# Kernel tuning notes

Measured on AMD Instinct MI355X. Metric: run time of the kernel, lower is better.

## Reference

```python
import jax, jax.numpy as jnp
import numpy as np
import math

TAU = 0.04
BIG = 100000.0


def _decay(initial, step, steps):
    de = initial * 0.75 * (1.0 + math.cos(math.pi * step / (steps / 2.0)))
    dm = initial * 0.75 * (1.0 + math.cos(math.pi * step / steps))
    e = de if step < steps / 2.0 else 0.0
    m = dm
    return e, m, 3.0 - e - m


def _normalize(x):
    return x / jnp.maximum(jnp.linalg.norm(x, axis=1, keepdims=True), 1e-12)


def _pdist(a2, b2, ab):
    # ||a_i||^2 + ||b_j||^2 - 2 a_i.b_j, clamped + sqrt (matches torch addmm_ path)
    return jnp.sqrt(jnp.clip(a2 + b2.T - 2.0 * ab, 1e-12, None))


def _row_extreme(masked, is_min):
    idx = jnp.argmin(masked, axis=1) if is_min else jnp.argmax(masked, axis=1)
    val = jnp.take_along_axis(masked, idx[:, None], axis=1)[:, 0]
    return val, idx


def _nanmedian(vals, mask):
    # lower-median over valid entries per row (torch.nanmedian semantics)
    k = mask.sum(axis=1)
    pos = jnp.maximum((k - 1) // 2, 0)
    order = jnp.argsort(jnp.where(mask, vals, jnp.inf), axis=1)
    med_idx = jnp.take_along_axis(order, pos[:, None], axis=1)[:, 0]
    med_val = jnp.take_along_axis(vals, med_idx[:, None], axis=1)[:, 0]
    med_val = jnp.where(k > 0, med_val, 0.0)  # NaN-median -> 0 as in source
    return med_val, med_idx


def _ce0(logits):
    # CrossEntropy with labels all 0 over 2 classes
    return jnp.mean(jax.nn.logsumexp(logits, axis=1) - logits[:, 0])


def _pair_loss(dist_vals_an, dist_vals_ap, an_t, ap_t):
    sg = jax.lax.stop_gradient
    w_an = jnp.clip(sg(an_t) - sg(dist_vals_an), 0.0, None)
    w_ap = jnp.clip(sg(dist_vals_ap) - sg(ap_t), 0.0, None)
    logits = jnp.stack([w_an * dist_vals_an / TAU, w_ap * dist_vals_ap / TAU], axis=1)
    return _ce0(logits)


def _forward(teacher_inputs, inputs, epoch):
    e, m, d = _decay(0.5, epoch, 240)
    t = _normalize(teacher_inputs)
    s = _normalize(inputs)
    t2 = jnp.sum(t * t, axis=1, keepdims=True)  # [n,1]
    s2 = jnp.sum(s * s, axis=1, keepdims=True)
    dist_t = _pdist(t2, t2, t @ t.T)            # teacher-teacher [n,n]
    dist = _pdist(t2, s2, t @ s.T)              # teacher-student [n,n]
    temp1 = jnp.diag(dist)[:, None]             # dist[i,i] broadcast over row i
    neg_mask = dist_t > temp1
    pos_mask = ~neg_mask

    gather_t = lambda idx: jnp.take_along_axis(dist_t, idx[:, None], axis=1)[:, 0]

    # hard mining (d-branch): nearest negative, farthest positive
    an_v, an_i = _row_extreme(jnp.where(neg_mask, dist, BIG), True)
    ap_v, ap_i = _row_extreme(jnp.where(pos_mask, dist, 0.0), False)
    loss_d = _pair_loss(an_v, ap_v, gather_t(an_i), gather_t(ap_i))

    # easy mining (e-branch): farthest negative, nearest positive
    an_ev, an_ei = _row_extreme(jnp.where(neg_mask, dist, 0.0), False)
    ap_ev, ap_ei = _row_extreme(jnp.where(pos_mask, dist, BIG), True)
    loss_e = _pair_loss(an_ev, ap_ev, gather_t(an_ei), gather_t(ap_ei))

    # median mining (m-branch)
    an_mv, an_mi = _nanmedian(dist, neg_mask)
    ap_mv, ap_mi = _nanmedian(dist, pos_mask)
    loss_m = _pair_loss(an_mv, ap_mv, gather_t(an_mi), gather_t(ap_mi))

    return loss_e * e + loss_m * m + loss_d * d


def setup_inputs() -> dict:
    key = jax.random.key(0)
    k1, k2 = jax.random.split(key)
    n, dim = 4096, 2048
    return {
        "teacher_inputs": jax.random.normal(k1, (n, dim), dtype=jnp.float32),
        "inputs": jax.random.normal(k2, (n, dim), dtype=jnp.float32),
        "epoch": 100,
    }


def reference(teacher_inputs, inputs, epoch):
    return _forward(teacher_inputs, inputs, epoch)
```

## Files before the change

### kernel.cpp

```cpp
#include <hip/hip_runtime.h>
#include <math.h>
#include <cfloat>
#include <climits>

#define NROW 4096
#define DIM  2048
#define BIGF 100000.0f
#define BIGU 0x47C35000u

typedef float  f32x4  __attribute__((ext_vector_type(4)));
typedef __bf16 bf16x8 __attribute__((ext_vector_type(8)));
typedef unsigned short us8v __attribute__((ext_vector_type(8)));

__device__ __forceinline__ unsigned short f2bf(float x) {
    unsigned u = __float_as_uint(x);
    u += 0x7fffu + ((u >> 16) & 1u);
    return (unsigned short)(u >> 16);
}
__device__ __forceinline__ float bf2f(unsigned short h) {
    return __uint_as_float(((unsigned)h) << 16);
}

__device__ __forceinline__ void gload16(const void* g, void* lds) {
    __builtin_amdgcn_global_load_lds(
        (const __attribute__((address_space(1))) unsigned int*)g,
        (__attribute__((address_space(3))) unsigned int*)lds,
        16, 0, 0);
}

__global__ __launch_bounds__(256) void k_norm_split(const float* __restrict__ in,
    unsigned short* __restrict__ hi, unsigned short* __restrict__ lo,
    float* __restrict__ sq)
{
    int row = blockIdx.x;
    int tid = threadIdx.x;
    const float4* rp = (const float4*)(in + (size_t)row * DIM);
    float4 v0 = rp[tid * 2 + 0];
    float4 v1 = rp[tid * 2 + 1];
    float ss = v0.x*v0.x + v0.y*v0.y + v0.z*v0.z + v0.w*v0.w
             + v1.x*v1.x + v1.y*v1.y + v1.z*v1.z + v1.w*v1.w;
    #pragma unroll
    for (int off = 32; off > 0; off >>= 1) ss += __shfl_down(ss, off, 64);
    __shared__ float wsum[4];
    __shared__ float s_den;
    if ((tid & 63) == 0) wsum[tid >> 6] = ss;
    __syncthreads();
    if (tid == 0) {
        float tot = wsum[0] + wsum[1] + wsum[2] + wsum[3];
        float den = fmaxf(sqrtf(tot), 1e-12f);
        s_den = den;
        sq[row] = tot / (den * den);
    }
    __syncthreads();
    float den = s_den;
    float xs[8];
    xs[0]=v0.x/den; xs[1]=v0.y/den; xs[2]=v0.z/den; xs[3]=v0.w/den;
    xs[4]=v1.x/den; xs[5]=v1.y/den; xs[6]=v1.z/den; xs[7]=v1.w/den;
    us8v hv, lv;
    #pragma unroll
    for (int j = 0; j < 8; ++j) {
        unsigned short h = f2bf(xs[j]);
        hv[j] = h;
        lv[j] = f2bf(xs[j] - bf2f(h));
    }
    *(us8v*)&hi[(size_t)row * DIM + tid * 8] = hv;
    *(us8v*)&lo[(size_t)row * DIM + tid * 8] = lv;
}

__global__ __launch_bounds__(256, 2) void k_gemm_mfma(
    const unsigned short* __restrict__ T1, const unsigned short* __restrict__ T2,
    const unsigned short* __restrict__ S1, const unsigned short* __restrict__ S2,
    const float* __restrict__ t2v, const float* __restrict__ s2v,
    float* __restrict__ distT, float* __restrict__ distS)
{
    __shared__ __align__(16) unsigned char smem[2][24576];

    int tid = threadIdx.x;

    int orig  = blockIdx.y * gridDim.x + blockIdx.x;
    int nwg   = gridDim.x * gridDim.y;
    int cpx   = nwg >> 3;
    int swz   = (orig & 7) * cpx + (orig >> 3);
    int bx    = swz % gridDim.x;
    int by    = swz / gridDim.x;
    int m0 = by * 128, n0 = bx * 128;

    int r0   = tid >> 2;
    int cs0  = (((tid & 3) ^ ((r0 >> 1) & 3)) << 4);
    unsigned ldst = (unsigned)tid * 16;

    int l  = tid & 63;
    int w  = tid >> 6;
    int wr = w >> 1, wc = w & 1;
    int lr = l & 15;
    int kc = l >> 4;

    f32x4 acc_t[4][4], acc_s[4][4];
    #pragma unroll
    for (int m = 0; m < 4; ++m)
        #pragma unroll
        for (int n = 0; n < 4; ++n) {
            acc_t[m][n] = (f32x4)0.0f;
            acc_s[m][n] = (f32x4)0.0f;
        }

    const int NT = 192;

    auto stage = [&](int tt, unsigned char* base) {
        int sg = tt >> 6;
        int k0 = (tt & 63) << 5;
        const char* pA  = (const char*)((sg == 2) ? T2 : T1);
        const char* pBt = (const char*)((sg == 1) ? T2 : T1);
        const char* pBs = (const char*)((sg == 1) ? S2 : S1);
        size_t gA0 = ((size_t)(m0 + r0)      * DIM + k0) * 2 + cs0;
        size_t gA1 = ((size_t)(m0 + 64 + r0) * DIM + k0) * 2 + cs0;
        size_t gB0 = ((size_t)(n0 + r0)      * DIM + k0) * 2 + cs0;
        size_t gB1 = ((size_t)(n0 + 64 + r0) * DIM + k0) * 2 + cs0;
        gload16(pA  + gA0, base + ldst);
        gload16(pA  + gA1, base + 4096  + ldst);
        gload16(pBt + gB0, base + 8192  + ldst);
        gload16(pBt + gB1, base + 12288 + ldst);
        gload16(pBs + gB0, base + 16384 + ldst);
        gload16(pBs + gB1, base + 20480 + ldst);
    };

    stage(0, smem[0]);
    __syncthreads();

    int cur = 0;
    for (int t = 0; t < NT; ++t) {
        if (t + 1 < NT) stage(t + 1, smem[cur ^ 1]);

        const unsigned char* base = smem[cur];
        bf16x8 a[4], btf[4], bsf[4];
        #pragma unroll
        for (int m = 0; m < 4; ++m) {
            int ra = wr * 64 + m * 16 + lr;
            int co = ((kc ^ ((ra >> 1) & 3)) << 4);
            a[m] = *(const bf16x8*)(base + ra * 64 + co);
        }
        #pragma unroll
        for (int n = 0; n < 4; ++n) {
            int rb = wc * 64 + n * 16 + lr;
            int co = ((kc ^ ((rb >> 1) & 3)) << 4);
            btf[n] = *(const bf16x8*)(base + 8192  + rb * 64 + co);
            bsf[n] = *(const bf16x8*)(base + 16384 + rb * 64 + co);
        }
        #pragma unroll
        for (int m = 0; m < 4; ++m)
            #pragma unroll
            for (int n = 0; n < 4; ++n) {
                acc_t[m][n] = __builtin_amdgcn_mfma_f32_16x16x32_bf16(
                    a[m], btf[n], acc_t[m][n], 0, 0, 0);
                acc_s[m][n] = __builtin_amdgcn_mfma_f32_16x16x32_bf16(
                    a[m], bsf[n], acc_s[m][n], 0, 0, 0);
            }

        __syncthreads();
        cur ^= 1;
    }

    int colb = n0 + wc * 64 + lr;
    int rowb = m0 + wr * 64 + (kc << 2);
    float t2row[4][4];
    #pragma unroll
    for (int m = 0; m < 4; ++m)
        #pragma unroll
        for (int r = 0; r < 4; ++r) t2row[m][r] = t2v[rowb + m * 16 + r];
    #pragma unroll
    for (int n = 0; n < 4; ++n) {
        int col = colb + n * 16;
        float t2c = t2v[col];
        float s2c = s2v[col];
        #pragma unroll
        for (int m = 0; m < 4; ++m) {
            f32x4 ct = acc_t[m][n];
            f32x4 cs = acc_s[m][n];
            int row = rowb + m * 16;
            #pragma unroll
            for (int r = 0; r < 4; ++r) {
                size_t o = (size_t)(row + r) * NROW + col;
                distT[o] = sqrtf(fmaxf(t2row[m][r] + t2c - 2.0f * ct[r], 1e-12f));
                distS[o] = sqrtf(fmaxf(t2row[m][r] + s2c - 2.0f * cs[r], 1e-12f));
            }
        }
    }
}

__device__ inline float pair_term(float an_v, float ap_v, float an_t, float ap_t)
{
    float w_an = fmaxf(an_t - an_v, 0.f);
    float w_ap = fmaxf(ap_v - ap_t, 0.f);
    float l0 = w_an * an_v / 0.04f;
    float l1 = w_ap * ap_v / 0.04f;
    float mx = fmaxf(l0, l1);
    return mx + logf(expf(l0 - mx) + expf(l1 - mx)) - l0;
}

__device__ __forceinline__ unsigned long long wred_min64(unsigned long long v) {
    #pragma unroll
    for (int o = 32; o > 0; o >>= 1) {
        unsigned long long x = __shfl_down(v, o, 64);
        v = (x < v) ? x : v;
    }
    return v;
}
__device__ __forceinline__ unsigned long long wred_max64(unsigned long long v) {
    #pragma unroll
    for (int o = 32; o > 0; o >>= 1) {
        unsigned long long x = __shfl_down(v, o, 64);
        v = (x > v) ? x : v;
    }
    return v;
}

__device__ void radix_select_reg(const unsigned u[16], unsigned negbits,
                                 unsigned selNeg, int rank,
                                 unsigned* hist, unsigned* s_wt, unsigned* s_sel,
                                 int tid, float& val, int& idx)
{
    unsigned prefix = 0;
    int r = rank;
    #pragma unroll
    for (int pass = 0; pass < 4; ++pass) {
        const int shift = 24 - pass * 8;
        hist[tid] = 0;
        __syncthreads();
        {
            unsigned curbin = 0xFFFFFFFFu, rl = 0;
            #pragma unroll
            for (int q = 0; q < 16; ++q) {
                unsigned key = (((negbits >> q) & 1u) == selNeg) ? u[q] : 0xFFFFFFFFu;
                bool match = (pass == 0) || ((key >> (shift + 8)) == (prefix >> (shift + 8)));
                if (match) {
                    unsigned b = (key >> shift) & 255u;
                    if (b == curbin) { rl++; }
                    else {
                        if (rl) atomicAdd(&hist[curbin], rl);
                        curbin = b; rl = 1;
                    }
                }
            }
            if (rl) atomicAdd(&hist[curbin], rl);
        }
        __syncthreads();
        unsigned h = hist[tid];
        unsigned incl = h;
        #pragma unroll
        for (int o = 1; o < 64; o <<= 1) {
            unsigned x = __shfl_up(incl, o, 64);
            if ((tid & 63) >= o) incl += x;
        }
        if ((tid & 63) == 63) s_wt[tid >> 6] = incl;
        __syncthreads();
        int wv = tid >> 6;
        unsigned base = 0;
        if (wv > 0) base += s_wt[0];
        if (wv > 1) base += s_wt[1];
        if (wv > 2) base += s_wt[2];
        incl += base;
        unsigned excl = incl - h;
        if ((unsigned)r >= excl && (unsigned)r < incl) {
            s_sel[0] = (unsigned)tid;
            s_sel[1] = (unsigned)r - excl;
        }
        __syncthreads();
        prefix |= s_sel[0] << shift;
        r = (int)s_sel[1];
        __syncthreads();
    }
    {
        unsigned cnt = 0;
        #pragma unroll
        for (int q = 0; q < 16; ++q) {
            unsigned key = (((negbits >> q) & 1u) == selNeg) ? u[q] : 0xFFFFFFFFu;
            if (key == prefix) cnt++;
        }
        hist[tid] = cnt;
        __syncthreads();
        unsigned incl = hist[tid];
        #pragma unroll
        for (int o = 1; o < 64; o <<= 1) {
            unsigned x = __shfl_up(incl, o, 64);
            if ((tid & 63) >= o) incl += x;
        }
        if ((tid & 63) == 63) s_wt[tid >> 6] = incl;
        __syncthreads();
        int wv = tid >> 6;
        unsigned base = 0;
        if (wv > 0) base += s_wt[0];
        if (wv > 1) base += s_wt[1];
        if (wv > 2) base += s_wt[2];
        incl += base;
        unsigned excl = incl - cnt;
        if ((unsigned)r >= excl && (unsigned)r < incl) {
            int need = r - (int)excl;
            #pragma unroll
            for (int q = 0; q < 16; ++q) {
                unsigned key = (((negbits >> q) & 1u) == selNeg) ? u[q] : 0xFFFFFFFFu;
                if (key == prefix) {
                    if (need == 0) { s_sel[0] = (unsigned)(tid * 16 + q); }
                    need--;
                }
            }
        }
        __syncthreads();
    }
    val = __uint_as_float(prefix);
    idx = (int)s_sel[0];
    __syncthreads();
}

__global__ __launch_bounds__(256) void k_rowstats(const float* __restrict__ distS,
    const float* __restrict__ distT, float* __restrict__ terms)
{
    __shared__ unsigned hist[256];
    __shared__ unsigned s_wt[4];
    __shared__ unsigned s_sel[2];
    __shared__ unsigned long long s_red[4][4];
    __shared__ int s_cw[4];
    __shared__ float s_t1;

    int i = blockIdx.x, tid = threadIdx.x;
    const float* dSrow = distS + (size_t)i * NROW;
    const float* dTrow = distT + (size_t)i * NROW;

    if (tid == 0) s_t1 = dSrow[i];

    float4 dv[4], tv[4];
    #pragma unroll
    for (int c = 0; c < 4; ++c) {
        dv[c] = *(const float4*)(dSrow + tid * 16 + c * 4);
        tv[c] = *(const float4*)(dTrow + tid * 16 + c * 4);
    }
    __syncthreads();
    float temp1 = s_t1;

    unsigned u[16];
    unsigned negbits = 0;
    #pragma unroll
    for (int c = 0; c < 4; ++c) {
        const float* dp = (const float*)&dv[c];
        const float* tp = (const float*)&tv[c];
        #pragma unroll
        for (int k = 0; k < 4; ++k) {
            int q = c * 4 + k;
            u[q] = __float_as_uint(dp[k]);
            if (tp[k] > temp1) negbits |= (1u << q);
        }
    }

    unsigned long long Pan  = ~0ull;
    unsigned long long Pap  = 0ull;
    unsigned long long Pane = 0ull;
    unsigned long long Pape = ~0ull;
    int cnt = 0;
    #pragma unroll
    for (int q = 0; q < 16; ++q) {
        unsigned j = (unsigned)(tid * 16 + q);
        unsigned neg = (negbits >> q) & 1u;
        cnt += (int)neg;
        unsigned kan  = neg ? u[q] : BIGU;
        unsigned kap  = neg ? 0u   : u[q];
        unsigned kane = neg ? u[q] : 0u;
        unsigned kape = neg ? BIGU : u[q];
        unsigned long long pan  = ((unsigned long long)kan  << 32) | j;
        unsigned long long pap  = ((unsigned long long)kap  << 32) | (0xFFFFFFFFu - j);
        unsigned long long pane = ((unsigned long long)kane << 32) | (0xFFFFFFFFu - j);
        unsigned long long pape = ((unsigned long long)kape << 32) | j;
        if (pan  < Pan)  Pan  = pan;
        if (pap  > Pap)  Pap  = pap;
        if (pane > Pane) Pane = pane;
        if (pape < Pape) Pape = pape;
    }
    Pan  = wred_min64(Pan);
    Pap  = wred_max64(Pap);
    Pane = wred_max64(Pane);
    Pape = wred_min64(Pape);
    #pragma unroll
    for (int o = 32; o > 0; o >>= 1) cnt += __shfl_down(cnt, o, 64);
    if ((tid & 63) == 0) {
        int wv = tid >> 6;
        s_red[0][wv] = Pan; s_red[1][wv] = Pap;
        s_red[2][wv] = Pane; s_red[3][wv] = Pape;
        s_cw[wv] = cnt;
    }
    __syncthreads();
    unsigned long long Ran = ~0ull, Rap = 0ull, Rane = 0ull, Rape = ~0ull;
    #pragma unroll
    for (int wv = 0; wv < 4; ++wv) {
        if (s_red[0][wv] < Ran)  Ran  = s_red[0][wv];
        if (s_red[1][wv] > Rap)  Rap  = s_red[1][wv];
        if (s_red[2][wv] > Rane) Rane = s_red[2][wv];
        if (s_red[3][wv] < Rape) Rape = s_red[3][wv];
    }
    int k_neg = s_cw[0] + s_cw[1] + s_cw[2] + s_cw[3];
    int k_pos = NROW - k_neg;

    float an_v  = __uint_as_float((unsigned)(Ran  >> 32)); int an_i  = (int)(Ran & 0xFFFFFFFFull);
    float ap_v  = __uint_as_float((unsigned)(Rap  >> 32)); int ap_i  = (int)(0xFFFFFFFFu - (unsigned)(Rap & 0xFFFFFFFFull));
    float ane_v = __uint_as_float((unsigned)(Rane >> 32)); int ane_i = (int)(0xFFFFFFFFu - (unsigned)(Rane & 0xFFFFFFFFull));
    float ape_v = __uint_as_float((unsigned)(Rape >> 32)); int ape_i = (int)(Rape & 0xFFFFFFFFull);

    __syncthreads();

    float mn_v; int mn_i;
    if (k_neg > 0) {
        radix_select_reg(u, negbits, 1u, (k_neg - 1) >> 1, hist, s_wt, s_sel, tid, mn_v, mn_i);
    } else { mn_v = 0.f; mn_i = 0; }
    float mp_v; int mp_i;
    if (k_pos > 0) {
        radix_select_reg(u, negbits, 0u, (k_pos - 1) >> 1, hist, s_wt, s_sel, tid, mp_v, mp_i);
    } else { mp_v = 0.f; mp_i = 0; }

    if (tid == 0) {
        float an_t  = dTrow[an_i];
        float ap_t  = dTrow[ap_i];
        float ane_t = dTrow[ane_i];
        float ape_t = dTrow[ape_i];
        float mn_t  = dTrow[mn_i];
        float mp_t  = dTrow[mp_i];
        terms[i]            = pair_term(an_v,  ap_v,  an_t,  ap_t);
        terms[NROW + i]     = pair_term(ane_v, ape_v, ane_t, ape_t);
        terms[2*NROW + i]   = pair_term(mn_v,  mp_v,  mn_t,  mp_t);
    }
}

__global__ __launch_bounds__(256) void k_finalize(const float* __restrict__ terms,
    const void* __restrict__ epoch_p, float* __restrict__ out)
{
    __shared__ float red[256];
    int tid = threadIdx.x;
    float s0 = 0.f, s1 = 0.f, s2 = 0.f;
    for (int j = tid; j < NROW; j += 256) {
        s0 += terms[j];
        s1 += terms[NROW + j];
        s2 += terms[2*NROW + j];
    }
    float tot[3];
    float sv[3] = {s0, s1, s2};
    for (int t = 0; t < 3; ++t) {
        red[tid] = sv[t];
        __syncthreads();
        for (int st = 128; st > 0; st >>= 1) {
            if (tid < st) red[tid] += red[tid + st];
            __syncthreads();
        }
        tot[t] = red[0];
        __syncthreads();
    }
    if (tid == 0) {
        int ei = *(const int*)epoch_p;
        double step;
        if (ei >= 0 && ei < 100000) step = (double)ei;
        else step = (double)(*(const float*)epoch_p);
        const double PI = 3.14159265358979323846;
        double de = 0.5 * 0.75 * (1.0 + cos(PI * step / 120.0));
        double dm = 0.5 * 0.75 * (1.0 + cos(PI * step / 240.0));
        double e = (step < 120.0) ? de : 0.0;
        double m = dm;
        double d = 3.0 - e - m;
        double loss_d = (double)tot[0] / (double)NROW;
        double loss_e = (double)tot[1] / (double)NROW;
        double loss_m = (double)tot[2] / (double)NROW;
        out[0] = (float)(loss_e * e + loss_m * m + loss_d * d);
    }
}

extern "C" void kernel_launch(void* const* d_in, const int* in_sizes, int n_in,
                              void* d_out, int out_size, void* d_ws, size_t ws_size,
                              hipStream_t stream)
{
    (void)in_sizes; (void)n_in; (void)out_size; (void)ws_size;
    const float* t_in = (const float*)d_in[0];
    const float* s_in = (const float*)d_in[1];
    const void*  epoch = d_in[2];
    float* out = (float*)d_out;

    char* ws = (char*)d_ws;
    size_t off = 0;
    unsigned short* T1 = (unsigned short*)(ws + off); off += (size_t)NROW * DIM * 2;
    unsigned short* T2 = (unsigned short*)(ws + off); off += (size_t)NROW * DIM * 2;
    unsigned short* S1 = (unsigned short*)(ws + off); off += (size_t)NROW * DIM * 2;
    unsigned short* S2 = (unsigned short*)(ws + off); off += (size_t)NROW * DIM * 2;
    float* t2v   = (float*)(ws + off); off += (size_t)NROW * 4;
    float* s2v   = (float*)(ws + off); off += (size_t)NROW * 4;
    float* distT = (float*)(ws + off); off += (size_t)NROW * NROW * 4;
    float* distS = (float*)(ws + off); off += (size_t)NROW * NROW * 4;
    float* terms = (float*)(ws + off); off += (size_t)3 * NROW * 4;

    k_norm_split<<<NROW, 256, 0, stream>>>(t_in, T1, T2, t2v);
    k_norm_split<<<NROW, 256, 0, stream>>>(s_in, S1, S2, s2v);
    k_gemm_mfma<<<dim3(32, 32), 256, 0, stream>>>(T1, T2, S1, S2, t2v, s2v, distT, distS);
    k_rowstats<<<NROW, 256, 0, stream>>>(distS, distT, terms);
    k_finalize<<<1, 256, 0, stream>>>(terms, epoch, out);
}
```

Baseline: 668.6 us.

## Triple-buffer GEMM LDS staging with partial vmcnt waits

Moves the fused teacher/student bf16 MFMA GEMM from double to triple buffering in LDS. It issues loads two tiles ahead and waits only on the older batch via s_waitcnt vmcnt(6) plus a raw barrier, instead of a full __syncthreads each iteration. Per-thread global offsets are also hoisted out of the staging lambda. The aim is to hide global-load latency behind MFMA work, at the cost of 72KB LDS per block, which may limit how many blocks fit per CU under launch_bounds(256,2).

```diff
diff --git a/kernel.cpp b/kernel.cpp
--- a/kernel.cpp
+++ b/kernel.cpp
@@ -73,7 +73,7 @@
     const float* __restrict__ t2v, const float* __restrict__ s2v,
     float* __restrict__ distT, float* __restrict__ distS)
 {
-    __shared__ __align__(16) unsigned char smem[2][24576];
+    __shared__ __align__(16) unsigned char smem[3][24576];
 
     int tid = threadIdx.x;
 
@@ -89,6 +89,11 @@
     int cs0  = (((tid & 3) ^ ((r0 >> 1) & 3)) << 4);
     unsigned ldst = (unsigned)tid * 16;
 
+    size_t offA0 = ((size_t)(m0 + r0)      * DIM) * 2 + cs0;
+    size_t offA1 = ((size_t)(m0 + 64 + r0) * DIM) * 2 + cs0;
+    size_t offB0 = ((size_t)(n0 + r0)      * DIM) * 2 + cs0;
+    size_t offB1 = ((size_t)(n0 + 64 + r0) * DIM) * 2 + cs0;
+
     int l  = tid & 63;
     int w  = tid >> 6;
     int wr = w >> 1, wc = w & 1;
@@ -108,30 +113,19 @@
 
     auto stage = [&](int tt, unsigned char* base) {
         int sg = tt >> 6;
-        int k0 = (tt & 63) << 5;
+        size_t kb = (size_t)(tt & 63) << 6;
         const char* pA  = (const char*)((sg == 2) ? T2 : T1);
         const char* pBt = (const char*)((sg == 1) ? T2 : T1);
         const char* pBs = (const char*)((sg == 1) ? S2 : S1);
-        size_t gA0 = ((size_t)(m0 + r0)      * DIM + k0) * 2 + cs0;
-        size_t gA1 = ((size_t)(m0 + 64 + r0) * DIM + k0) * 2 + cs0;
-        size_t gB0 = ((size_t)(n0 + r0)      * DIM + k0) * 2 + cs0;
-        size_t gB1 = ((size_t)(n0 + 64 + r0) * DIM + k0) * 2 + cs0;
-        gload16(pA  + gA0, base + ldst);
-        gload16(pA  + gA1, base + 4096  + ldst);
-        gload16(pBt + gB0, base + 8192  + ldst);
-        gload16(pBt + gB1, base + 12288 + ldst);
-        gload16(pBs + gB0, base + 16384 + ldst);
-        gload16(pBs + gB1, base + 20480 + ldst);
+        gload16(pA  + offA0 + kb, base + ldst);
+        gload16(pA  + offA1 + kb, base + 4096  + ldst);
+        gload16(pBt + offB0 + kb, base + 8192  + ldst);
+        gload16(pBt + offB1 + kb, base + 12288 + ldst);
+        gload16(pBs + offB0 + kb, base + 16384 + ldst);
+        gload16(pBs + offB1 + kb, base + 20480 + ldst);
     };
 
-    stage(0, smem[0]);
-    __syncthreads();
-
-    int cur = 0;
-    for (int t = 0; t < NT; ++t) {
-        if (t + 1 < NT) stage(t + 1, smem[cur ^ 1]);
-
-        const unsigned char* base = smem[cur];
+    auto compute = [&](const unsigned char* base) {
         bf16x8 a[4], btf[4], bsf[4];
         #pragma unroll
         for (int m = 0; m < 4; ++m) {
@@ -155,10 +149,28 @@
                 acc_s[m][n] = __builtin_amdgcn_mfma_f32_16x16x32_bf16(
                     a[m], bsf[n], acc_s[m][n], 0, 0, 0);
             }
-
-        __syncthreads();
-        cur ^= 1;
-    }
+    };
+
+    unsigned char* pa = smem[0];
+    unsigned char* pb = smem[1];
+    unsigned char* pc = smem[2];
+
+    stage(0, pa);
+    stage(1, pb);
+    asm volatile("s_waitcnt vmcnt(6)" ::: "memory");
+    __builtin_amdgcn_s_barrier();
+
+    for (int t = 0; t < NT - 2; ++t) {
+        stage(t + 2, pc);
+        compute(pa);
+        asm volatile("s_waitcnt vmcnt(6)" ::: "memory");
+        __builtin_amdgcn_s_barrier();
+        unsigned char* tmp = pa; pa = pb; pb = pc; pc = tmp;
+    }
+    compute(pa);
+    asm volatile("s_waitcnt vmcnt(0)" ::: "memory");
+    __builtin_amdgcn_s_barrier();
+    compute(pb);
 
     int colb = n0 + wc * 64 + lr;
     int rowb = m0 + wr * 64 + (kc << 2);
```

After: 746.5 us. 1.12x slower.

## Interleave dual median radix selects with early exit to small candidate sort

Applied to the files above, without the earlier changes.

The two per-row median radix selections (negative and positive sets) now run interleaved in the same passes, which shares the barriers and scans between them. Each selection also stops once the selected bucket holds at most 256 elements and finishes with an in-shared-memory rank sort of the packed (value, index) candidates. The two normalization launches are merged into one grid of twice the size. Together these aim to cut barrier count and passes in the row-stats kernel and one launch, at the cost of more shared memory and code complexity. Tie-breaking relies on the packed index in the candidate key.

```diff
diff --git a/kernel.cpp b/kernel.cpp
--- a/kernel.cpp
+++ b/kernel.cpp
@@ -28,11 +28,20 @@
         16, 0, 0);
 }
 
-__global__ __launch_bounds__(256) void k_norm_split(const float* __restrict__ in,
-    unsigned short* __restrict__ hi, unsigned short* __restrict__ lo,
-    float* __restrict__ sq)
+__global__ __launch_bounds__(256) void k_norm_split(
+    const float* __restrict__ t_in, const float* __restrict__ s_in,
+    unsigned short* __restrict__ T1, unsigned short* __restrict__ T2,
+    unsigned short* __restrict__ S1, unsigned short* __restrict__ S2,
+    float* __restrict__ t2v, float* __restrict__ s2v)
 {
-    int row = blockIdx.x;
+    int b   = blockIdx.x;
+    int row = b & (NROW - 1);
+    bool isS = b >= NROW;
+    const float* in = isS ? s_in : t_in;
+    unsigned short* hi = isS ? S1 : T1;
+    unsigned short* lo = isS ? S2 : T2;
+    float* sq = isS ? s2v : t2v;
+
     int tid = threadIdx.x;
     const float4* rp = (const float4*)(in + (size_t)row * DIM);
     float4 v0 = rp[tid * 2 + 0];
@@ -214,109 +223,15 @@
     return v;
 }
 
-__device__ void radix_select_reg(const unsigned u[16], unsigned negbits,
-                                 unsigned selNeg, int rank,
-                                 unsigned* hist, unsigned* s_wt, unsigned* s_sel,
-                                 int tid, float& val, int& idx)
-{
-    unsigned prefix = 0;
-    int r = rank;
-    #pragma unroll
-    for (int pass = 0; pass < 4; ++pass) {
-        const int shift = 24 - pass * 8;
-        hist[tid] = 0;
-        __syncthreads();
-        {
-            unsigned curbin = 0xFFFFFFFFu, rl = 0;
-            #pragma unroll
-            for (int q = 0; q < 16; ++q) {
-                unsigned key = (((negbits >> q) & 1u) == selNeg) ? u[q] : 0xFFFFFFFFu;
-                bool match = (pass == 0) || ((key >> (shift + 8)) == (prefix >> (shift + 8)));
-                if (match) {
-                    unsigned b = (key >> shift) & 255u;
-                    if (b == curbin) { rl++; }
-                    else {
-                        if (rl) atomicAdd(&hist[curbin], rl);
-                        curbin = b; rl = 1;
-                    }
-                }
-            }
-            if (rl) atomicAdd(&hist[curbin], rl);
-        }
-        __syncthreads();
-        unsigned h = hist[tid];
-        unsigned incl = h;
-        #pragma unroll
-        for (int o = 1; o < 64; o <<= 1) {
-            unsigned x = __shfl_up(incl, o, 64);
-            if ((tid & 63) >= o) incl += x;
-        }
-        if ((tid & 63) == 63) s_wt[tid >> 6] = incl;
-        __syncthreads();
-        int wv = tid >> 6;
-        unsigned base = 0;
-        if (wv > 0) base += s_wt[0];
-        if (wv > 1) base += s_wt[1];
-        if (wv > 2) base += s_wt[2];
-        incl += base;
-        unsigned excl = incl - h;
-        if ((unsigned)r >= excl && (unsigned)r < incl) {
-            s_sel[0] = (unsigned)tid;
-            s_sel[1] = (unsigned)r - excl;
-        }
-        __syncthreads();
-        prefix |= s_sel[0] << shift;
-        r = (int)s_sel[1];
-        __syncthreads();
-    }
-    {
-        unsigned cnt = 0;
-        #pragma unroll
-        for (int q = 0; q < 16; ++q) {
-            unsigned key = (((negbits >> q) & 1u) == selNeg) ? u[q] : 0xFFFFFFFFu;
-            if (key == prefix) cnt++;
-        }
-        hist[tid] = cnt;
-        __syncthreads();
-        unsigned incl = hist[tid];
-        #pragma unroll
-        for (int o = 1; o < 64; o <<= 1) {
-            unsigned x = __shfl_up(incl, o, 64);
-            if ((tid & 63) >= o) incl += x;
-        }
-        if ((tid & 63) == 63) s_wt[tid >> 6] = incl;
-        __syncthreads();
-        int wv = tid >> 6;
-        unsigned base = 0;
-        if (wv > 0) base += s_wt[0];
-        if (wv > 1) base += s_wt[1];
-        if (wv > 2) base += s_wt[2];
-        incl += base;
-        unsigned excl = incl - cnt;
-        if ((unsigned)r >= excl && (unsigned)r < incl) {
-            int need = r - (int)excl;
-            #pragma unroll
-            for (int q = 0; q < 16; ++q) {
-                unsigned key = (((negbits >> q) & 1u) == selNeg) ? u[q] : 0xFFFFFFFFu;
-                if (key == prefix) {
-                    if (need == 0) { s_sel[0] = (unsigned)(tid * 16 + q); }
-                    need--;
-                }
-            }
-        }
-        __syncthreads();
-    }
-    val = __uint_as_float(prefix);
-    idx = (int)s_sel[0];
-    __syncthreads();
-}
-
 __global__ __launch_bounds__(256) void k_rowstats(const float* __restrict__ distS,
     const float* __restrict__ distT, float* __restrict__ terms)
 {
-    __shared__ unsigned hist[256];
-    __shared__ unsigned s_wt[4];
-    __shared__ unsigned s_sel[2];
+    __shared__ unsigned histN[256], histP[256];
+    __shared__ unsigned s_wtN[4], s_wtP[4];
+    __shared__ unsigned selN[2], selP[2];
+    __shared__ unsigned long long cand[256];
+    __shared__ unsigned ccnt;
+    __shared__ unsigned long long s_res;
     __shared__ unsigned long long s_red[4][4];
     __shared__ int s_cw[4];
     __shared__ float s_t1;
@@ -404,14 +319,197 @@
 
     __syncthreads();
 
-    float mn_v; int mn_i;
-    if (k_neg > 0) {
-        radix_select_reg(u, negbits, 1u, (k_neg - 1) >> 1, hist, s_wt, s_sel, tid, mn_v, mn_i);
-    } else { mn_v = 0.f; mn_i = 0; }
-    float mp_v; int mp_i;
-    if (k_pos > 0) {
-        radix_select_reg(u, negbits, 0u, (k_pos - 1) >> 1, hist, s_wt, s_sel, tid, mp_v, mp_i);
-    } else { mp_v = 0.f; mp_i = 0; }
+    int rN = (k_neg > 0) ? ((k_neg - 1) >> 1) : -1;
+    int rP = (k_pos > 0) ? ((k_pos - 1) >> 1) : -1;
+    bool doneN = (rN < 0), doneP = (rP < 0);
+    bool candN = false, candP = false, ordN = false, ordP = false;
+    int  shN = 0, shP = 0;
+    unsigned prefN = 0, prefP = 0;
+
+    for (int pass = 0; pass < 4; ++pass) {
+        if (doneN && doneP) break;
+        const int shift = 24 - pass * 8;
+        if (!doneN) histN[tid] = 0;
+        if (!doneP) histP[tid] = 0;
+        __syncthreads();
+        if (!doneN) {
+            unsigned curbin = 0xFFFFFFFFu, rl = 0;
+            #pragma unroll
+            for (int q = 0; q < 16; ++q) {
+                unsigned key = ((negbits >> q) & 1u) ? u[q] : 0xFFFFFFFFu;
+                bool match = (pass == 0) || ((key >> (shift + 8)) == (prefN >> (shift + 8)));
+                if (match) {
+                    unsigned b = (key >> shift) & 255u;
+                    if (b == curbin) rl++;
+                    else { if (rl) atomicAdd(&histN[curbin], rl); curbin = b; rl = 1; }
+                }
+            }
+            if (rl) atomicAdd(&histN[curbin], rl);
+        }
+        if (!doneP) {
+            unsigned curbin = 0xFFFFFFFFu, rl = 0;
+            #pragma unroll
+            for (int q = 0; q < 16; ++q) {
+                unsigned key = ((negbits >> q) & 1u) ? 0xFFFFFFFFu : u[q];
+                bool match = (pass == 0) || ((key >> (shift + 8)) == (prefP >> (shift + 8)));
+                if (match) {
+                    unsigned b = (key >> shift) & 255u;
+                    if (b == curbin) rl++;
+                    else { if (rl) atomicAdd(&histP[curbin], rl); curbin = b; rl = 1; }
+                }
+            }
+            if (rl) atomicAdd(&histP[curbin], rl);
+        }
+        __syncthreads();
+        unsigned hN = doneN ? 0u : histN[tid];
+        unsigned hP = doneP ? 0u : histP[tid];
+        unsigned iN = hN, iP = hP;
+        #pragma unroll
+        for (int o = 1; o < 64; o <<= 1) {
+            unsigned xN = __shfl_up(iN, o, 64);
+            unsigned xP = __shfl_up(iP, o, 64);
+            if ((tid & 63) >= o) { iN += xN; iP += xP; }
+        }
+        if ((tid & 63) == 63) { s_wtN[tid >> 6] = iN; s_wtP[tid >> 6] = iP; }
+        __syncthreads();
+        {
+            int wv = tid >> 6;
+            unsigned bN = 0, bP = 0;
+            if (wv > 0) { bN += s_wtN[0]; bP += s_wtP[0]; }
+            if (wv > 1) { bN += s_wtN[1]; bP += s_wtP[1]; }
+            if (wv > 2) { bN += s_wtN[2]; bP += s_wtP[2]; }
+            iN += bN; iP += bP;
+        }
+        if (!doneN) {
+            unsigned e = iN - hN;
+            if ((unsigned)rN >= e && (unsigned)rN < iN) { selN[0] = (unsigned)tid; selN[1] = (unsigned)rN - e; }
+        }
+        if (!doneP) {
+            unsigned e = iP - hP;
+            if ((unsigned)rP >= e && (unsigned)rP < iP) { selP[0] = (unsigned)tid; selP[1] = (unsigned)rP - e; }
+        }
+        __syncthreads();
+        if (!doneN) {
+            unsigned b = selN[0]; prefN |= b << shift; rN = (int)selN[1];
+            unsigned hb = histN[b];
+            if (hb <= 256u)      { candN = true; doneN = true; shN = shift; }
+            else if (shift == 0) { ordN  = true; doneN = true; }
+        }
+        if (!doneP) {
+            unsigned b = selP[0]; prefP |= b << shift; rP = (int)selP[1];
+            unsigned hb = histP[b];
+            if (hb <= 256u)      { candP = true; doneP = true; shP = shift; }
+            else if (shift == 0) { ordP  = true; doneP = true; }
+        }
+        __syncthreads();
+    }
+
+    float mn_v = 0.f; int mn_i = 0;
+    float mp_v = 0.f; int mp_i = 0;
+
+    if (candN) {
+        if (tid == 0) ccnt = 0;
+        __syncthreads();
+        #pragma unroll
+        for (int q = 0; q < 16; ++q) {
+            unsigned key = ((negbits >> q) & 1u) ? u[q] : 0xFFFFFFFFu;
+            if ((key >> shN) == (prefN >> shN)) {
+                unsigned p = atomicAdd(&ccnt, 1u);
+                cand[p] = ((unsigned long long)u[q] << 12) | (unsigned)(tid * 16 + q);
+            }
+        }
+        __syncthreads();
+        int c = (int)ccnt;
+        if (tid < c) {
+            unsigned long long my = cand[tid];
+            int rk = 0;
+            for (int t2 = 0; t2 < c; ++t2) rk += (cand[t2] < my) ? 1 : 0;
+            if (rk == rN) s_res = my;
+        }
+        __syncthreads();
+        mn_v = __uint_as_float((unsigned)(s_res >> 12));
+        mn_i = (int)(s_res & 0xFFFull);
+        __syncthreads();
+    } else if (ordN) {
+        unsigned cq = 0;
+        #pragma unroll
+        for (int q = 0; q < 16; ++q) {
+            unsigned key = ((negbits >> q) & 1u) ? u[q] : 0xFFFFFFFFu;
+            if (key == prefN) cq++;
+        }
+        histN[tid] = cq;
+        __syncthreads();
+        unsigned h = histN[tid], incl = h;
+        #pragma unroll
+        for (int o = 1; o < 64; o <<= 1) { unsigned x = __shfl_up(incl, o, 64); if ((tid & 63) >= o) incl += x; }
+        if ((tid & 63) == 63) s_wtN[tid >> 6] = incl;
+        __syncthreads();
+        { int wv = tid >> 6; unsigned b = 0; if (wv > 0) b += s_wtN[0]; if (wv > 1) b += s_wtN[1]; if (wv > 2) b += s_wtN[2]; incl += b; }
+        unsigned excl = incl - h;
+        if ((unsigned)rN >= excl && (unsigned)rN < incl) {
+            int need = rN - (int)excl;
+            #pragma unroll
+            for (int q = 0; q < 16; ++q) {
+                unsigned key = ((negbits >> q) & 1u) ? u[q] : 0xFFFFFFFFu;
+                if (key == prefN) { if (need == 0) selN[0] = (unsigned)(tid * 16 + q); need--; }
+            }
+        }
+        __syncthreads();
+        mn_v = __uint_as_float(prefN);
+        mn_i = (int)selN[0];
+        __syncthreads();
+    }
+
+    if (candP) {
+        if (tid == 0) ccnt = 0;
+        __syncthreads();
+        #pragma unroll
+        for (int q = 0; q < 16; ++q) {
+            unsigned key = ((negbits >> q) & 1u) ? 0xFFFFFFFFu : u[q];
+            if ((key >> shP) == (prefP >> shP)) {
+                unsigned p = atomicAdd(&ccnt, 1u);
+                cand[p] = ((unsigned long long)u[q] << 12) | (unsigned)(tid * 16 + q);
+            }
+        }
+        __syncthreads();
+        int c = (int)ccnt;
+        if (tid < c) {
+            unsigned long long my = cand[tid];
+            int rk = 0;
+            for (int t2 = 0; t2 < c; ++t2) rk += (cand[t2] < my) ? 1 : 0;
+            if (rk == rP) s_res = my;
+        }
+        __syncthreads();
+        mp_v = __uint_as_float((unsigned)(s_res >> 12));
+        mp_i = (int)(s_res & 0xFFFull);
+    } else if (ordP) {
+        unsigned cq = 0;
+        #pragma unroll
+        for (int q = 0; q < 16; ++q) {
+            unsigned key = ((negbits >> q) & 1u) ? 0xFFFFFFFFu : u[q];
+            if (key == prefP) cq++;
+        }
+        histP[tid] = cq;
+        __syncthreads();
+        unsigned h = histP[tid], incl = h;
+        #pragma unroll
+        for (int o = 1; o < 64; o <<= 1) { unsigned x = __shfl_up(incl, o, 64); if ((tid & 63) >= o) incl += x; }
+        if ((tid & 63) == 63) s_wtP[tid >> 6] = incl;
+        __syncthreads();
+        { int wv = tid >> 6; unsigned b = 0; if (wv > 0) b += s_wtP[0]; if (wv > 1) b += s_wtP[1]; if (wv > 2) b += s_wtP[2]; incl += b; }
+        unsigned excl = incl - h;
+        if ((unsigned)rP >= excl && (unsigned)rP < incl) {
+            int need = rP - (int)excl;
+            #pragma unroll
+            for (int q = 0; q < 16; ++q) {
+                unsigned key = ((negbits >> q) & 1u) ? 0xFFFFFFFFu : u[q];
+                if (key == prefP) { if (need == 0) selP[0] = (unsigned)(tid * 16 + q); need--; }
+            }
+        }
+        __syncthreads();
+        mp_v = __uint_as_float(prefP);
+        mp_i = (int)selP[0];
+    }
 
     if (tid == 0) {
         float an_t  = dTrow[an_i];
@@ -489,8 +587,7 @@
     float* distS = (float*)(ws + off); off += (size_t)NROW * NROW * 4;
     float* terms = (float*)(ws + off); off += (size_t)3 * NROW * 4;
 
-    k_norm_split<<<NROW, 256, 0, stream>>>(t_in, T1, T2, t2v);
-    k_norm_split<<<NROW, 256, 0, stream>>>(s_in, S1, S2, s2v);
+    k_norm_split<<<2 * NROW, 256, 0, stream>>>(t_in, s_in, T1, T2, S1, S2, t2v, s2v);
     k_gemm_mfma<<<dim3(32, 32), 256, 0, stream>>>(T1, T2, S1, S2, t2v, s2v, distT, distS);
     k_rowstats<<<NROW, 256, 0, stream>>>(distS, distT, terms);
     k_finalize<<<1, 256, 0, stream>>>(terms, epoch, out);
```

Result: faster. 624.3 us (-6.6%).
